# Kernel tuning notes

Measured on AMD Instinct MI355X. Metric: run time of the kernel, lower is better.

## Reference

```python
import jax, jax.numpy as jnp
import numpy as np

DIM, HEADS = 512, 8
CH = DIM // HEADS  # 64
WINDOWS = [3, 5, 7]
HEAD_SPLITS = [2, 3, 3]  # heads per conv window group (sums to HEADS)


def setup_inputs() -> dict:
    key = jax.random.key(0)
    ks = jax.random.split(key, 12)
    B, N = 8, 4096
    s = 0.02
    inp = {
        'x':  jax.random.normal(ks[0], (B, N, DIM), jnp.float32),
        'mx': jax.random.normal(ks[1], (B, N, DIM), jnp.float32),
        'Wqkv': jax.random.normal(ks[2], (3 * DIM, DIM), jnp.float32) * s,
        'Wproj': jax.random.normal(ks[3], (DIM, DIM), jnp.float32) * s,
        'bproj': jax.random.normal(ks[4], (DIM,), jnp.float32) * s,
        'Wmix': jax.random.normal(ks[5], (CH, 2 * CH), jnp.float32) * s,
        'bmix': jax.random.normal(ks[6], (CH,), jnp.float32) * s,
    }
    for i, (w, hs) in enumerate(zip(WINDOWS, HEAD_SPLITS)):
        gc = hs * CH  # depthwise channels in this group
        inp[f'conv_w{w}'] = jax.random.normal(ks[7 + i], (gc, 1, w, w), jnp.float32) * s
        inp[f'conv_b{w}'] = jnp.zeros((gc,), jnp.float32)
    inp['H'] = 64
    inp['W'] = 64
    return inp


def _dwconv(x, w, b, k):
    # x: [B, C, H, W]; depthwise conv, 'same' padding
    out = jax.lax.conv_general_dilated(
        x, w, window_strides=(1, 1), padding=[(k // 2, k // 2)] * 2,
        feature_group_count=x.shape[1],
        dimension_numbers=('NCHW', 'OIHW', 'NCHW'))
    return out + b[None, :, None, None]


def _crpe(q, v, H, W, conv_ws, conv_bs):
    # q, v: [B, h, N, Ch] with N == H*W
    B, h, N, ch = q.shape
    v_img = v.transpose(0, 1, 3, 2).reshape(B, h * ch, H, W)
    bounds = np.cumsum([0] + [s * ch for s in HEAD_SPLITS])
    outs = [_dwconv(v_img[:, bounds[i]:bounds[i + 1]], conv_ws[i], conv_bs[i], WINDOWS[i])
            for i in range(len(WINDOWS))]
    conv_v = jnp.concatenate(outs, axis=1).reshape(B, h, ch, H * W).transpose(0, 1, 3, 2)
    return q * conv_v


def reference(x, mx, Wqkv, Wproj, bproj, Wmix, bmix,
              conv_w3, conv_w5, conv_w7, conv_b3, conv_b5, conv_b7, H, W):
    B, N, C = x.shape
    scale = CH ** -0.5
    # qkv for x: [B,N,3C] -> [3,B,h,N,Ch]
    qkv = (x @ Wqkv.T).reshape(B, N, 3, HEADS, CH).transpose(2, 0, 3, 1, 4)
    q, k, v = qkv[0], qkv[1], qkv[2]
    # only the q-part of qkv(mx) is used
    mq = (mx @ Wqkv[:C].T).reshape(B, N, HEADS, CH).transpose(0, 2, 1, 3)
    # mixed q (fed to crpe only)
    q_mix = jnp.concatenate([mq, q], axis=-1) @ Wmix.T + bmix
    # factorized attention: softmax over sequence dim of k
    k_sm = jax.nn.softmax(k, axis=2)
    kv = jnp.einsum('bhnk,bhnv->bhkv', k_sm, v)          # [B,h,Ch,Ch]
    factor_att = jnp.einsum('bhnk,bhkv->bhnv', mq, kv)    # [B,h,N,Ch]
    crpe = _crpe(q_mix, v, H, W,
                 (conv_w3, conv_w5, conv_w7), (conv_b3, conv_b5, conv_b7))
    out = scale * factor_att + crpe
    out = out.transpose(0, 2, 1, 3).reshape(B, N, C)
    return out @ Wproj.T + bproj
```

## Files before the change

kernel.cpp:

```cpp
#include <hip/hip_runtime.h>
#include <hip/hip_bf16.h>

#define MROWS 32768
#define NSEQ 4096
#define KDIM 512

typedef short sh8 __attribute__((ext_vector_type(8)));
typedef float fx4 __attribute__((ext_vector_type(4)));

__device__ __forceinline__ unsigned short f2bf(float f) {
  union { float f; unsigned u; } v; v.f = f;
  unsigned r = v.u + 0x7FFFu + ((v.u >> 16) & 1u);
  return (unsigned short)(r >> 16);
}
__device__ __forceinline__ float bf2f(unsigned short u) {
  union { unsigned u; float f; } v; v.u = ((unsigned)u) << 16;
  return v.f;
}

__device__ __forceinline__ void gload16(const unsigned short* g, unsigned short* l) {
  __builtin_amdgcn_global_load_lds(
      (const __attribute__((address_space(1))) unsigned int*)g,
      (__attribute__((address_space(3))) unsigned int*)l, 16, 0, 0);
}

template<bool A_BF16, bool OUT_BF16, bool HAS_BIAS, bool TWO, bool PER_B2, int NXL>
__global__ __launch_bounds__(256) void gemm_bf16(
    const void* Av, const unsigned short* __restrict__ W,
    const void* A2v, const unsigned short* __restrict__ W2,
    const float* __restrict__ bias, void* Co, int Nn) {
  __shared__ unsigned short As[128 * 64];
  __shared__ unsigned short Bs[128 * 64];
  const int tid = threadIdx.x;
  const int lane = tid & 63, wv = tid >> 6;
  const int wr = wv >> 1, wc = wv & 1;
  const int nwg = gridDim.x;
  const int lid = (blockIdx.x & 7) * (nwg >> 3) + (blockIdx.x >> 3);
  const int bx = lid & ((1 << NXL) - 1);
  const int by = lid >> NXL;
  const int fr = lane & 15, fg = lane >> 4;
  const int srow = lane >> 3;
  const int sphys = lane & 7;
  fx4 acc[4][4] = {};
#pragma unroll
  for (int pass = 0; pass < (TWO ? 2 : 1); ++pass) {
    const unsigned short* Wp = (TWO && pass) ? W2 : W;
    if (TWO && pass && PER_B2) Wp += (size_t)(by >> 5) * (512 * 512);
    const void* Ap = (TWO && pass) ? A2v : Av;
    for (int k0 = 0; k0 < KDIM; k0 += 64) {
#pragma unroll
      for (int l = 0; l < 4; ++l) {
        int rb = wv * 4 + l;
        int r = rb * 8 + srow;
        int clog = sphys ^ (r & 7);
        gload16(Wp + (size_t)(bx * 128 + r) * KDIM + k0 + clog * 8, &Bs[rb * 512]);
      }
      if constexpr (A_BF16) {
        const unsigned short* Ab = (const unsigned short*)Ap;
#pragma unroll
        for (int l = 0; l < 4; ++l) {
          int rb = wv * 4 + l;
          int r = rb * 8 + srow;
          int clog = sphys ^ (r & 7);
          gload16(Ab + (size_t)(by * 128 + r) * KDIM + k0 + clog * 8, &As[rb * 512]);
        }
      } else {
        const float* Af = (const float*)Ap;
#pragma unroll
        for (int s = 0; s < 4; ++s) {
          int u = s * 256 + tid;
          int r = u >> 3, cp = u & 7;
          int clog = cp ^ (r & 7);
          const float* src = Af + (size_t)(by * 128 + r) * KDIM + k0 + clog * 8;
          float4 v0 = *reinterpret_cast<const float4*>(src);
          float4 v1 = *reinterpret_cast<const float4*>(src + 4);
          uint4 o;
          o.x = (unsigned)f2bf(v0.x) | ((unsigned)f2bf(v0.y) << 16);
          o.y = (unsigned)f2bf(v0.z) | ((unsigned)f2bf(v0.w) << 16);
          o.z = (unsigned)f2bf(v1.x) | ((unsigned)f2bf(v1.y) << 16);
          o.w = (unsigned)f2bf(v1.z) | ((unsigned)f2bf(v1.w) << 16);
          *reinterpret_cast<uint4*>(&As[r * 64 + cp * 8]) = o;
        }
      }
      __syncthreads();
#pragma unroll
      for (int ks = 0; ks < 2; ++ks) {
        sh8 a[4], b[4];
#pragma unroll
        for (int m = 0; m < 4; ++m) {
          int r = wr * 64 + m * 16 + fr;
          int p = (ks * 4 + fg) ^ (r & 7);
          a[m] = *reinterpret_cast<const sh8*>(&As[r * 64 + p * 8]);
        }
#pragma unroll
        for (int n = 0; n < 4; ++n) {
          int r = wc * 64 + n * 16 + fr;
          int p = (ks * 4 + fg) ^ (r & 7);
          b[n] = *reinterpret_cast<const sh8*>(&Bs[r * 64 + p * 8]);
        }
#pragma unroll
        for (int m = 0; m < 4; ++m)
#pragma unroll
          for (int n = 0; n < 4; ++n)
            acc[m][n] = __builtin_amdgcn_mfma_f32_16x16x32_bf16(a[m], b[n], acc[m][n], 0, 0, 0);
      }
      __syncthreads();
    }
  }
  unsigned short* Cb = (unsigned short*)Co;
  float* Cf = (float*)Co;
#pragma unroll
  for (int n = 0; n < 4; ++n) {
    int col = bx * 128 + wc * 64 + n * 16 + fr;
    float bb = 0.f;
    if constexpr (HAS_BIAS) bb = bias[col];
#pragma unroll
    for (int m = 0; m < 4; ++m) {
#pragma unroll
      for (int j = 0; j < 4; ++j) {
        int row = by * 128 + wr * 64 + m * 16 + fg * 4 + j;
        float val = acc[m][n][j] + bb;
        if constexpr (OUT_BF16)
          Cb[(size_t)row * Nn + col] = f2bf(val);
        else
          Cf[(size_t)row * Nn + col] = val;
      }
    }
  }
}

__global__ __launch_bounds__(256) void cvt_bf16(
    const float* __restrict__ src, unsigned short* __restrict__ dst, int n8) {
  int i = blockIdx.x * 256 + threadIdx.x;
  if (i >= n8) return;
  float4 v0 = *reinterpret_cast<const float4*>(src + (size_t)i * 8);
  float4 v1 = *reinterpret_cast<const float4*>(src + (size_t)i * 8 + 4);
  uint4 o;
  o.x = (unsigned)f2bf(v0.x) | ((unsigned)f2bf(v0.y) << 16);
  o.y = (unsigned)f2bf(v0.z) | ((unsigned)f2bf(v0.w) << 16);
  o.z = (unsigned)f2bf(v1.x) | ((unsigned)f2bf(v1.y) << 16);
  o.w = (unsigned)f2bf(v1.z) | ((unsigned)f2bf(v1.w) << 16);
  *reinterpret_cast<uint4*>(dst + (size_t)i * 8) = o;
}

__global__ __launch_bounds__(256) void eff_weights(
    const float* __restrict__ Wqkv, const float* __restrict__ Wmix,
    const float* __restrict__ bmix,
    unsigned short* __restrict__ W1, unsigned short* __restrict__ W2,
    float* __restrict__ bmixfull) {
  int r = blockIdx.x;
  int h = r >> 6, j = r & 63;
  int t = threadIdx.x;
  if (t == 0) bmixfull[r] = bmix[j];
  float a10 = 0.f, a11 = 0.f, a20 = 0.f, a21 = 0.f;
  for (int i = 0; i < 64; ++i) {
    float w1 = Wmix[j * 128 + i], w2 = Wmix[j * 128 + 64 + i];
    const float* wr = Wqkv + (size_t)(h * 64 + i) * KDIM;
    a10 = fmaf(w1, wr[t], a10);
    a11 = fmaf(w1, wr[t + 256], a11);
    a20 = fmaf(w2, wr[t], a20);
    a21 = fmaf(w2, wr[t + 256], a21);
  }
  W1[(size_t)r * KDIM + t] = f2bf(a10);
  W1[(size_t)r * KDIM + t + 256] = f2bf(a11);
  W2[(size_t)r * KDIM + t] = f2bf(a20);
  W2[(size_t)r * KDIM + t + 256] = f2bf(a21);
}

__global__ __launch_bounds__(256) void wtrans(
    const float* __restrict__ w3, const float* __restrict__ w5,
    const float* __restrict__ w7,
    float* __restrict__ wT3, float* __restrict__ wT5, float* __restrict__ wT7) {
  int i = blockIdx.x * 256 + threadIdx.x;
  if (i < 1152) {
    int ti = i >> 7, c = i & 127;
    wT3[i] = w3[c * 9 + ti];
  } else if (i < 5952) {
    int j = i - 1152;
    int ti = j / 192, c = j - ti * 192;
    wT5[j] = w5[c * 25 + ti];
  } else {
    int j = i - 5952;
    int ti = j / 192, c = j - ti * 192;
    wT7[j] = w7[c * 49 + ti];
  }
}

__global__ __launch_bounds__(256) void zero_colsum(float* __restrict__ p) {
  int i = (blockIdx.x * 256 + threadIdx.x) * 4;
  *reinterpret_cast<float4*>(p + i) = make_float4(0.f, 0.f, 0.f, 0.f);
}

__global__ __launch_bounds__(256) void kv_mfma(
    const unsigned short* __restrict__ kvmat,
    float* __restrict__ kvpart, float* __restrict__ colsum) {
  __shared__ unsigned short eK[64][40];
  __shared__ unsigned short eV[64][40];
  __shared__ float cw[4][64];
  int t = threadIdx.x;
  int split = blockIdx.x & 7;
  int bh = blockIdx.x >> 3;
  int h = bh & 7, b = bh >> 3;
  int lane = t & 63, wv = t >> 6;
  int wr = wv >> 1, wc = wv & 1;
  int fr = lane & 15, fg = lane >> 4;
  int cg = t & 7, nl = t >> 3;
  const unsigned short* kb = kvmat + (size_t)b * NSEQ * 1024 + h * 64 + cg * 8;
  const unsigned short* vb = kb + 512;
  int colS = nl ^ ((cg & 3) << 3);
  fx4 acc[2][2] = {};
  float csum[8] = {};
  for (int n0 = split * 512; n0 < split * 512 + 512; n0 += 32) {
    size_t off = (size_t)(n0 + nl) * 1024;
    sh8 k8 = *reinterpret_cast<const sh8*>(kb + off);
    sh8 v8 = *reinterpret_cast<const sh8*>(vb + off);
#pragma unroll
    for (int j = 0; j < 8; ++j) {
      float e = __expf(bf2f((unsigned short)k8[j]));
      csum[j] += e;
      eK[cg * 8 + j][colS] = f2bf(e);
      eV[cg * 8 + j][colS] = (unsigned short)v8[j];
    }
    __syncthreads();
    sh8 a[2], bb[2];
#pragma unroll
    for (int m = 0; m < 2; ++m) {
      int r = wr * 32 + m * 16 + fr;
      int c8 = (fg ^ ((r >> 3) & 3)) * 8;
      a[m] = *reinterpret_cast<const sh8*>(&eK[r][c8]);
    }
#pragma unroll
    for (int n = 0; n < 2; ++n) {
      int r = wc * 32 + n * 16 + fr;
      int c8 = (fg ^ ((r >> 3) & 3)) * 8;
      bb[n] = *reinterpret_cast<const sh8*>(&eV[r][c8]);
    }
#pragma unroll
    for (int m = 0; m < 2; ++m)
#pragma unroll
      for (int n = 0; n < 2; ++n)
        acc[m][n] = __builtin_amdgcn_mfma_f32_16x16x32_bf16(a[m], bb[n], acc[m][n], 0, 0, 0);
    __syncthreads();
  }
  float* kvp = kvpart + (size_t)split * 64 * 4096 + (size_t)bh * 4096;
#pragma unroll
  for (int m = 0; m < 2; ++m)
#pragma unroll
    for (int n = 0; n < 2; ++n)
#pragma unroll
      for (int j = 0; j < 4; ++j) {
        int row = wr * 32 + m * 16 + fg * 4 + j;
        int col = wc * 32 + n * 16 + fr;
        kvp[row * 64 + col] = acc[m][n][j];
      }
#pragma unroll
  for (int j = 0; j < 8; ++j) {
    float v = csum[j];
    v += __shfl_xor(v, 8);
    v += __shfl_xor(v, 16);
    v += __shfl_xor(v, 32);
    csum[j] = v;
  }
  if (lane < 8) {
#pragma unroll
    for (int j = 0; j < 8; ++j) cw[wv][lane * 8 + j] = csum[j];
  }
  __syncthreads();
  if (t < 64) {
    float s = cw[0][t] + cw[1][t] + cw[2][t] + cw[3][t];
    atomicAdd(&colsum[b * 512 + h * 64 + t], s);
  }
}

__global__ __launch_bounds__(256) void kv_reduce(
    const float* __restrict__ kvpart, float* __restrict__ kvbuf) {
  int i = (blockIdx.x * 256 + threadIdx.x) * 4;
  float4 s = make_float4(0.f, 0.f, 0.f, 0.f);
#pragma unroll
  for (int sp = 0; sp < 8; ++sp) {
    float4 v = *reinterpret_cast<const float4*>(kvpart + (size_t)sp * 262144 + i);
    s.x += v.x; s.y += v.y; s.z += v.z; s.w += v.w;
  }
  *reinterpret_cast<float4*>(kvbuf + i) = s;
}

__global__ __launch_bounds__(256) void wproj_eff(
    const float* __restrict__ kvbuf, const float* __restrict__ Wproj,
    const float* __restrict__ colsum, unsigned short* __restrict__ Wb) {
  int bid = blockIdx.x;
  int jt = bid & 15, h = (bid >> 4) & 7, b = bid >> 7;
  int j0 = jt * 32;
  __shared__ float kvs[64][65];
  __shared__ float wps[32][64];
  int t = threadIdx.x;
  const float* kvsrc = kvbuf + (size_t)(b * 8 + h) * 4096;
  for (int i = t; i < 4096; i += 256) kvs[i >> 6][i & 63] = kvsrc[i];
  for (int i = t; i < 2048; i += 256)
    wps[i >> 6][i & 63] = Wproj[(size_t)(j0 + (i >> 6)) * 512 + h * 64 + (i & 63)];
  __syncthreads();
  int ck = t & 63, jl = t >> 6;
  float rs = 0.125f / colsum[b * 512 + h * 64 + ck];
  float acc[8] = {};
  for (int ch = 0; ch < 64; ++ch) {
    float kvv = kvs[ck][ch];
#pragma unroll
    for (int g = 0; g < 8; ++g)
      acc[g] = fmaf(kvv, wps[jl * 8 + g][ch], acc[g]);
  }
#pragma unroll
  for (int g = 0; g < 8; ++g)
    Wb[((size_t)b * 512 + j0 + jl * 8 + g) * 512 + h * 64 + ck] = f2bf(rs * acc[g]);
}

template<int KW, int C0, int CG, int TPB>
__global__ __launch_bounds__(TPB) void conv_crpe(
    const unsigned short* __restrict__ kvmat,
    unsigned short* __restrict__ qmixb,
    const float* __restrict__ wT, const float* __restrict__ bias) {
  constexpr int SLOTS = CG / 8;
  constexpr int ROWS_PB = TPB / SLOTS;
  constexpr int P = KW / 2;
  int t = threadIdx.x;
  int row_local = t / SLOTS;
  int slot = t - row_local * SLOTS;
  int row = blockIdx.x * ROWS_PB + row_local;
  int n = row & 4095, b = row >> 12;
  int y = n >> 6, x = n & 63;
  int cl = slot * 8;
  float acc[8] = {};
  const unsigned short* vb =
      kvmat + (size_t)b * NSEQ * 1024 + 512 + C0 + cl;
#pragma unroll
  for (int dy = 0; dy < KW; ++dy) {
    int yy = y + dy - P;
    if ((unsigned)yy >= 64u) continue;
#pragma unroll
    for (int dx = 0; dx < KW; ++dx) {
      int xq = x + dx - P;
      if ((unsigned)xq >= 64u) continue;
      sh8 v8 = *reinterpret_cast<const sh8*>(vb + (size_t)(yy * 64 + xq) * 1024);
      const float* wp = wT + (dy * KW + dx) * CG + cl;
      float4 w0 = *reinterpret_cast<const float4*>(wp);
      float4 w1 = *reinterpret_cast<const float4*>(wp + 4);
      acc[0] = fmaf(w0.x, bf2f((unsigned short)v8[0]), acc[0]);
      acc[1] = fmaf(w0.y, bf2f((unsigned short)v8[1]), acc[1]);
      acc[2] = fmaf(w0.z, bf2f((unsigned short)v8[2]), acc[2]);
      acc[3] = fmaf(w0.w, bf2f((unsigned short)v8[3]), acc[3]);
      acc[4] = fmaf(w1.x, bf2f((unsigned short)v8[4]), acc[4]);
      acc[5] = fmaf(w1.y, bf2f((unsigned short)v8[5]), acc[5]);
      acc[6] = fmaf(w1.z, bf2f((unsigned short)v8[6]), acc[6]);
      acc[7] = fmaf(w1.w, bf2f((unsigned short)v8[7]), acc[7]);
    }
  }
  float4 b0 = *reinterpret_cast<const float4*>(bias + cl);
  float4 b1 = *reinterpret_cast<const float4*>(bias + cl + 4);
  unsigned short* qp = qmixb + (size_t)row * 512 + C0 + cl;
  sh8 qm = *reinterpret_cast<const sh8*>(qp);
  sh8 out;
  out[0] = (short)f2bf(bf2f((unsigned short)qm[0]) * (acc[0] + b0.x));
  out[1] = (short)f2bf(bf2f((unsigned short)qm[1]) * (acc[1] + b0.y));
  out[2] = (short)f2bf(bf2f((unsigned short)qm[2]) * (acc[2] + b0.z));
  out[3] = (short)f2bf(bf2f((unsigned short)qm[3]) * (acc[3] + b0.w));
  out[4] = (short)f2bf(bf2f((unsigned short)qm[4]) * (acc[4] + b1.x));
  out[5] = (short)f2bf(bf2f((unsigned short)qm[5]) * (acc[5] + b1.y));
  out[6] = (short)f2bf(bf2f((unsigned short)qm[6]) * (acc[6] + b1.z));
  out[7] = (short)f2bf(bf2f((unsigned short)qm[7]) * (acc[7] + b1.w));
  *reinterpret_cast<sh8*>(qp) = out;
}

extern "C" void kernel_launch(void* const* d_in, const int* in_sizes, int n_in,
                              void* d_out, int out_size, void* d_ws, size_t ws_size,
                              hipStream_t stream) {
  const float* x     = (const float*)d_in[0];
  const float* mx    = (const float*)d_in[1];
  const float* Wqkv  = (const float*)d_in[2];
  const float* Wproj = (const float*)d_in[3];
  const float* bproj = (const float*)d_in[4];
  const float* Wmix  = (const float*)d_in[5];
  const float* bmix  = (const float*)d_in[6];
  const float* w3    = (const float*)d_in[7];
  const float* b3    = (const float*)d_in[8];
  const float* w5    = (const float*)d_in[9];
  const float* b5    = (const float*)d_in[10];
  const float* w7    = (const float*)d_in[11];
  const float* b7    = (const float*)d_in[12];

  unsigned short* kvmat = (unsigned short*)d_out;

  char* wsp = (char*)d_ws;
  auto carve = [&wsp](size_t bytes) {
    char* p = wsp;
    wsp += (bytes + 255) & ~(size_t)255;
    return p;
  };
  unsigned short* mqb    = (unsigned short*)carve((size_t)MROWS * 512 * 2);
  unsigned short* qmixb  = (unsigned short*)carve((size_t)MROWS * 512 * 2);
  unsigned short* Wqkvb  = (unsigned short*)carve((size_t)1536 * 512 * 2);
  unsigned short* Wprojb = (unsigned short*)carve((size_t)512 * 512 * 2);
  unsigned short* W1b    = (unsigned short*)carve((size_t)512 * 512 * 2);
  unsigned short* W2b    = (unsigned short*)carve((size_t)512 * 512 * 2);
  float* bmixf  = (float*)carve(512 * 4);
  float* kvbuf  = (float*)carve(8 * 8 * 64 * 64 * 4);
  float* colsum = (float*)carve(4096 * 4);
  float* wT3    = (float*)carve(9 * 128 * 4);
  float* wT5    = (float*)carve(25 * 192 * 4);
  float* wT7    = (float*)carve(49 * 192 * 4);
  float* kvpart = (float*)carve((size_t)8 * 64 * 4096 * 4);
  unsigned short* Wb = (unsigned short*)carve((size_t)8 * 512 * 512 * 2);

  dim3 blk(256);
  eff_weights<<<dim3(512), blk, 0, stream>>>(Wqkv, Wmix, bmix, W1b, W2b, bmixf);
  wtrans<<<dim3(60), blk, 0, stream>>>(w3, w5, w7, wT3, wT5, wT7);
  cvt_bf16<<<dim3(384), blk, 0, stream>>>(Wqkv, Wqkvb, 1536 * 512 / 8);
  cvt_bf16<<<dim3(128), blk, 0, stream>>>(Wproj, Wprojb, 512 * 512 / 8);
  gemm_bf16<false, true, false, false, false, 3><<<dim3(2048), blk, 0, stream>>>(
      x, Wqkvb + (size_t)512 * 512, nullptr, nullptr, nullptr, kvmat, 1024);
  gemm_bf16<false, true, false, false, false, 2><<<dim3(1024), blk, 0, stream>>>(
      mx, Wqkvb, nullptr, nullptr, nullptr, mqb, 512);
  gemm_bf16<false, true, true, true, false, 2><<<dim3(1024), blk, 0, stream>>>(
      mx, W1b, x, W2b, bmixf, qmixb, 512);
  zero_colsum<<<dim3(4), blk, 0, stream>>>(colsum);
  kv_mfma<<<dim3(512), blk, 0, stream>>>(kvmat, kvpart, colsum);
  kv_reduce<<<dim3(256), blk, 0, stream>>>(kvpart, kvbuf);
  wproj_eff<<<dim3(1024), blk, 0, stream>>>(kvbuf, Wproj, colsum, Wb);
  conv_crpe<3, 0, 128, 256><<<dim3(2048), dim3(256), 0, stream>>>(kvmat, qmixb, wT3, b3);
  conv_crpe<5, 128, 192, 192><<<dim3(4096), dim3(192), 0, stream>>>(kvmat, qmixb, wT5, b5);
  conv_crpe<7, 320, 192, 192><<<dim3(4096), dim3(192), 0, stream>>>(kvmat, qmixb, wT7, b7);
  gemm_bf16<true, false, true, true, true, 2><<<dim3(1024), blk, 0, stream>>>(
      qmixb, Wprojb, mqb, Wb, bproj, d_out, 512);
}
```

Baseline: 551.7 us.

## Pre-convert activations to bf16 and halve GEMM K-tile to 32

```diff
diff --git a/kernel.cpp b/kernel.cpp
--- a/kernel.cpp
+++ b/kernel.cpp
@@ -29,8 +29,8 @@
     const void* Av, const unsigned short* __restrict__ W,
     const void* A2v, const unsigned short* __restrict__ W2,
     const float* __restrict__ bias, void* Co, int Nn) {
-  __shared__ unsigned short As[128 * 64];
-  __shared__ unsigned short Bs[128 * 64];
+  __shared__ unsigned short As[128 * 32];
+  __shared__ unsigned short Bs[128 * 32];
   const int tid = threadIdx.x;
   const int lane = tid & 63, wv = tid >> 6;
   const int wr = wv >> 1, wc = wv & 1;
@@ -39,38 +39,36 @@
   const int bx = lid & ((1 << NXL) - 1);
   const int by = lid >> NXL;
   const int fr = lane & 15, fg = lane >> 4;
-  const int srow = lane >> 3;
-  const int sphys = lane & 7;
   fx4 acc[4][4] = {};
 #pragma unroll
   for (int pass = 0; pass < (TWO ? 2 : 1); ++pass) {
     const unsigned short* Wp = (TWO && pass) ? W2 : W;
     if (TWO && pass && PER_B2) Wp += (size_t)(by >> 5) * (512 * 512);
     const void* Ap = (TWO && pass) ? A2v : Av;
-    for (int k0 = 0; k0 < KDIM; k0 += 64) {
-#pragma unroll
-      for (int l = 0; l < 4; ++l) {
-        int rb = wv * 4 + l;
-        int r = rb * 8 + srow;
-        int clog = sphys ^ (r & 7);
-        gload16(Wp + (size_t)(bx * 128 + r) * KDIM + k0 + clog * 8, &Bs[rb * 512]);
+    for (int k0 = 0; k0 < KDIM; k0 += 32) {
+#pragma unroll
+      for (int l = 0; l < 2; ++l) {
+        int chunk = wv * 2 + l;
+        int r = chunk * 16 + (lane >> 2);
+        int clog = (lane & 3) ^ (r & 3);
+        gload16(Wp + (size_t)(bx * 128 + r) * KDIM + k0 + clog * 8, &Bs[chunk * 512]);
       }
       if constexpr (A_BF16) {
         const unsigned short* Ab = (const unsigned short*)Ap;
 #pragma unroll
-        for (int l = 0; l < 4; ++l) {
-          int rb = wv * 4 + l;
-          int r = rb * 8 + srow;
-          int clog = sphys ^ (r & 7);
-          gload16(Ab + (size_t)(by * 128 + r) * KDIM + k0 + clog * 8, &As[rb * 512]);
+        for (int l = 0; l < 2; ++l) {
+          int chunk = wv * 2 + l;
+          int r = chunk * 16 + (lane >> 2);
+          int clog = (lane & 3) ^ (r & 3);
+          gload16(Ab + (size_t)(by * 128 + r) * KDIM + k0 + clog * 8, &As[chunk * 512]);
         }
       } else {
         const float* Af = (const float*)Ap;
 #pragma unroll
-        for (int s = 0; s < 4; ++s) {
+        for (int s = 0; s < 2; ++s) {
           int u = s * 256 + tid;
-          int r = u >> 3, cp = u & 7;
-          int clog = cp ^ (r & 7);
+          int r = u >> 2, cp = u & 3;
+          int clog = cp ^ (r & 3);
           const float* src = Af + (size_t)(by * 128 + r) * KDIM + k0 + clog * 8;
           float4 v0 = *reinterpret_cast<const float4*>(src);
           float4 v1 = *reinterpret_cast<const float4*>(src + 4);
@@ -79,31 +77,28 @@
           o.y = (unsigned)f2bf(v0.z) | ((unsigned)f2bf(v0.w) << 16);
           o.z = (unsigned)f2bf(v1.x) | ((unsigned)f2bf(v1.y) << 16);
           o.w = (unsigned)f2bf(v1.z) | ((unsigned)f2bf(v1.w) << 16);
-          *reinterpret_cast<uint4*>(&As[r * 64 + cp * 8]) = o;
+          *reinterpret_cast<uint4*>(&As[r * 32 + cp * 8]) = o;
         }
       }
       __syncthreads();
-#pragma unroll
-      for (int ks = 0; ks < 2; ++ks) {
-        sh8 a[4], b[4];
-#pragma unroll
-        for (int m = 0; m < 4; ++m) {
-          int r = wr * 64 + m * 16 + fr;
-          int p = (ks * 4 + fg) ^ (r & 7);
-          a[m] = *reinterpret_cast<const sh8*>(&As[r * 64 + p * 8]);
-        }
-#pragma unroll
-        for (int n = 0; n < 4; ++n) {
-          int r = wc * 64 + n * 16 + fr;
-          int p = (ks * 4 + fg) ^ (r & 7);
-          b[n] = *reinterpret_cast<const sh8*>(&Bs[r * 64 + p * 8]);
-        }
-#pragma unroll
-        for (int m = 0; m < 4; ++m)
-#pragma unroll
-          for (int n = 0; n < 4; ++n)
-            acc[m][n] = __builtin_amdgcn_mfma_f32_16x16x32_bf16(a[m], b[n], acc[m][n], 0, 0, 0);
-      }
+      sh8 a[4], b[4];
+#pragma unroll
+      for (int m = 0; m < 4; ++m) {
+        int r = wr * 64 + m * 16 + fr;
+        int p = fg ^ (r & 3);
+        a[m] = *reinterpret_cast<const sh8*>(&As[r * 32 + p * 8]);
+      }
+#pragma unroll
+      for (int n = 0; n < 4; ++n) {
+        int r = wc * 64 + n * 16 + fr;
+        int p = fg ^ (r & 3);
+        b[n] = *reinterpret_cast<const sh8*>(&Bs[r * 32 + p * 8]);
+      }
+#pragma unroll
+      for (int m = 0; m < 4; ++m)
+#pragma unroll
+        for (int n = 0; n < 4; ++n)
+          acc[m][n] = __builtin_amdgcn_mfma_f32_16x16x32_bf16(a[m], b[n], acc[m][n], 0, 0, 0);
       __syncthreads();
     }
   }
@@ -407,18 +402,32 @@
   float* wT7    = (float*)carve(49 * 192 * 4);
   float* kvpart = (float*)carve((size_t)8 * 64 * 4096 * 4);
   unsigned short* Wb = (unsigned short*)carve((size_t)8 * 512 * 512 * 2);
+  unsigned short* xb  = (unsigned short*)carve((size_t)MROWS * 512 * 2);
+  unsigned short* mxb = (unsigned short*)carve((size_t)MROWS * 512 * 2);
+  const bool use16 = (size_t)(wsp - (char*)d_ws) <= ws_size;
 
   dim3 blk(256);
   eff_weights<<<dim3(512), blk, 0, stream>>>(Wqkv, Wmix, bmix, W1b, W2b, bmixf);
   wtrans<<<dim3(60), blk, 0, stream>>>(w3, w5, w7, wT3, wT5, wT7);
   cvt_bf16<<<dim3(384), blk, 0, stream>>>(Wqkv, Wqkvb, 1536 * 512 / 8);
   cvt_bf16<<<dim3(128), blk, 0, stream>>>(Wproj, Wprojb, 512 * 512 / 8);
-  gemm_bf16<false, true, false, false, false, 3><<<dim3(2048), blk, 0, stream>>>(
-      x, Wqkvb + (size_t)512 * 512, nullptr, nullptr, nullptr, kvmat, 1024);
-  gemm_bf16<false, true, false, false, false, 2><<<dim3(1024), blk, 0, stream>>>(
-      mx, Wqkvb, nullptr, nullptr, nullptr, mqb, 512);
-  gemm_bf16<false, true, true, true, false, 2><<<dim3(1024), blk, 0, stream>>>(
-      mx, W1b, x, W2b, bmixf, qmixb, 512);
+  if (use16) {
+    cvt_bf16<<<dim3(8192), blk, 0, stream>>>(x, xb, MROWS * 512 / 8);
+    cvt_bf16<<<dim3(8192), blk, 0, stream>>>(mx, mxb, MROWS * 512 / 8);
+    gemm_bf16<true, true, false, false, false, 3><<<dim3(2048), blk, 0, stream>>>(
+        xb, Wqkvb + (size_t)512 * 512, nullptr, nullptr, nullptr, kvmat, 1024);
+    gemm_bf16<true, true, false, false, false, 2><<<dim3(1024), blk, 0, stream>>>(
+        mxb, Wqkvb, nullptr, nullptr, nullptr, mqb, 512);
+    gemm_bf16<true, true, true, true, false, 2><<<dim3(1024), blk, 0, stream>>>(
+        mxb, W1b, xb, W2b, bmixf, qmixb, 512);
+  } else {
+    gemm_bf16<false, true, false, false, false, 3><<<dim3(2048), blk, 0, stream>>>(
+        x, Wqkvb + (size_t)512 * 512, nullptr, nullptr, nullptr, kvmat, 1024);
+    gemm_bf16<false, true, false, false, false, 2><<<dim3(1024), blk, 0, stream>>>(
+        mx, Wqkvb, nullptr, nullptr, nullptr, mqb, 512);
+    gemm_bf16<false, true, true, true, false, 2><<<dim3(1024), blk, 0, stream>>>(
+        mx, W1b, x, W2b, bmixf, qmixb, 512);
+  }
   zero_colsum<<<dim3(4), blk, 0, stream>>>(colsum);
   kv_mfma<<<dim3(512), blk, 0, stream>>>(kvmat, kvpart, colsum);
   kv_reduce<<<dim3(256), blk, 0, stream>>>(kvpart, kvbuf);
```

New measurement: 511.4 us. 7.3% less time.
